# Optimization experiments

Measured on AMD Instinct MI355X. Metric: run time of the kernel, lower is better.

The kernel has to match this reference:

```python
import jax, jax.numpy as jnp
import numpy as np

D = 768          # emb_dim (BERT hidden size)
N_DOM = 9        # domain_num
N_EXP = 6        # num_expert (per-domain)
N_SH = 4         # num_shared_expert
N_TOT = N_EXP + N_SH  # total experts seen by the gate
B = 2048


def _p(key, shape, scale=0.02):
    return jax.random.normal(key, shape, dtype=jnp.float32) * scale


def setup_inputs() -> dict:
    key = jax.random.key(0)
    ks = jax.random.split(key, 32)
    inp = {
        "content_pooled": jax.random.normal(ks[0], (B, D), dtype=jnp.float32),
        "ftr_pooled": jax.random.normal(ks[1], (B, D), dtype=jnp.float32),
        "category": jax.random.randint(ks[2], (B,), 0, N_DOM, dtype=jnp.int64),
        "domain_emb": _p(ks[3], (N_DOM, D), 1.0),
    }
    # per-domain expert stacks: Linear(D,D)-SiLU-Linear(D,D), for content (c) and ftr (f)
    for pre, base in (("c", 4), ("f", 12)):
        inp[pre + "W1"] = _p(ks[base + 0], (N_DOM, N_EXP, D, D))
        inp[pre + "b1"] = jnp.zeros((N_DOM, N_EXP, D), jnp.float32)
        inp[pre + "W2"] = _p(ks[base + 1], (N_DOM, N_EXP, D, D))
        inp[pre + "b2"] = jnp.zeros((N_DOM, N_EXP, D), jnp.float32)
        # shared experts: Linear(D,D)-SiLU-Linear(D,D)
        inp[pre + "sW1"] = _p(ks[base + 2], (N_SH, D, D))
        inp[pre + "sb1"] = jnp.zeros((N_SH, D), jnp.float32)
        inp[pre + "sW2"] = _p(ks[base + 3], (N_SH, D, D))
        inp[pre + "sb2"] = jnp.zeros((N_SH, D), jnp.float32)
        # per-domain enhanced gates: Linear(2D,D)-SiLU-Linear(D,N_TOT), temperature scalar per domain
        inp[pre + "gW1"] = _p(ks[base + 4], (N_DOM, 2 * D, D))
        inp[pre + "gb1"] = jnp.zeros((N_DOM, D), jnp.float32)
        inp[pre + "gW2"] = _p(ks[base + 5], (N_DOM, D, N_TOT))
        inp[pre + "gb2"] = jnp.zeros((N_DOM, N_TOT), jnp.float32)
        inp[pre + "temp"] = jnp.ones((N_DOM,), jnp.float32)
    return inp


def _moe_branch(x, category, domain_emb, W1, b1, W2, b2,
                sW1, sb1, sW2, sb2, gW1, gb1, gW2, gb2, temp):
    # x: [B, D]; category: [B] int in [0, N_DOM)
    demb = domain_emb[category]                           # [B, D]
    g_in = jnp.concatenate([demb, x], axis=-1)            # [B, 2D]
    # gate computed for all domains, then per-example domain selected
    gh = jax.nn.silu(jnp.einsum("bx,nxh->bnh", g_in, gW1) + gb1)      # [B, 9, D]
    logits = jnp.einsum("bnh,nhe->bne", gh, gW2) + gb2                 # [B, 9, 10]
    t = jax.nn.softplus(temp) + 1e-4                                    # positive temperature
    gates_all = jax.nn.softmax(logits / t[None, :, None], axis=-1)
    gates = jnp.take_along_axis(gates_all, category[:, None, None], axis=1)[:, 0]  # [B, 10]
    # per-domain experts for all domains (grouped GEMM form), then select domain
    h1 = jax.nn.silu(jnp.einsum("bd,nedh->bneh", x, W1) + b1)          # [B, 9, 6, D]
    e_all = jnp.einsum("bneh,nehd->bned", h1, W2) + b2                 # [B, 9, 6, D]
    e_dom = jnp.take_along_axis(e_all, category[:, None, None, None], axis=1)[:, 0]  # [B, 6, D]
    # shared experts
    hs = jax.nn.silu(jnp.einsum("bd,edh->beh", x, sW1) + sb1)          # [B, 4, D]
    e_sh = jnp.einsum("beh,ehd->bed", hs, sW2) + sb2                   # [B, 4, D]
    experts = jnp.concatenate([e_dom, e_sh], axis=1)                   # [B, 10, D]
    return jnp.einsum("be,bed->bd", gates, experts)                    # [B, D]


def reference(content_pooled, ftr_pooled, category, domain_emb,
              cW1, cb1, cW2, cb2, csW1, csb1, csW2, csb2,
              cgW1, cgb1, cgW2, cgb2, ctemp,
              fW1, fb1, fW2, fb2, fsW1, fsb1, fsW2, fsb2,
              fgW1, fgb1, fgW2, fgb2, ftemp):
    c_out = _moe_branch(content_pooled, category, domain_emb,
                        cW1, cb1, cW2, cb2, csW1, csb1, csW2, csb2,
                        cgW1, cgb1, cgW2, cgb2, ctemp)
    f_out = _moe_branch(ftr_pooled, category, domain_emb,
                        fW1, fb1, fW2, fb2, fsW1, fsb1, fsW2, fsb2,
                        fgW1, fgb1, fgW2, fgb2, ftemp)
    return jnp.concatenate([c_out, f_out], axis=-1)  # [B, 2D]
```

## Files before the change

### kernel.cpp

```cpp
#include <hip/hip_runtime.h>

#define D_ 768
#define B_ 2048
#define NDOM 9
#define NTOT 10
#define MT 128
#define KT 32
#define KI1 (D_ / KT)

#define E2   589824ull
#define E2G  1179648ull
#define OFF_WT2 31850496ull
#define OFF_SW1 63700992ull
#define OFF_SW2 66060288ull
#define OFF_GW1 68419584ull
#define ZWE     79036416ull

typedef _Float16 f16;
typedef _Float16 f16x8 __attribute__((ext_vector_type(8)));
typedef float f32x4 __attribute__((ext_vector_type(4)));

typedef const __attribute__((address_space(1))) void gas_void;
typedef __attribute__((address_space(3))) void las_void;

__device__ __forceinline__ void gload16(const f16* g, f16* l) {
  __builtin_amdgcn_global_load_lds((gas_void*)g, (las_void*)l, 16, 0, 0);
}

__global__ __launch_bounds__(256) void bucket_kernel(const int* cat32, int* perm,
                                                     int* off, int* cnt, int* dom) {
  __shared__ int scnt[NDOM], soff[NDOM], scur[NDOM];
  __shared__ int odd_nz;
  int t = threadIdx.x;
  if (t == 0) odd_nz = 0;
  if (t < NDOM) scnt[t] = 0;
  __syncthreads();
  int loc = 0;
  for (int i = t; i < B_; i += 256)
    if ((i & 1) && cat32[i] != 0) loc = 1;
  if (loc) atomicOr(&odd_nz, 1);
  __syncthreads();
  int strd = odd_nz ? 1 : 2;
  for (int i = t; i < B_; i += 256) atomicAdd(&scnt[cat32[i * strd]], 1);
  __syncthreads();
  if (t == 0) { int a = 0; for (int n = 0; n < NDOM; n++) { soff[n] = a; a += scnt[n]; } }
  __syncthreads();
  if (t < NDOM) { scur[t] = soff[t]; off[t] = soff[t]; cnt[t] = scnt[t]; }
  __syncthreads();
  for (int i = t; i < B_; i += 256) {
    int n = cat32[i * strd];
    int pos = atomicAdd(&scur[n], 1);
    perm[pos] = i;
    dom[pos] = n;
  }
}

__global__ __launch_bounds__(256) void cvt_perm_kernel(const float* src, f16* dst,
                                                       const int* perm, int n8) {
  int i = blockIdx.x * 256 + threadIdx.x;
  if (i >= n8) return;
  int row = i / (D_ / 8), c8 = i % (D_ / 8);
  int srow = perm[row];
  const f32x4* s = (const f32x4*)(src + (size_t)srow * D_ + c8 * 8);
  f32x4 a = s[0], b = s[1];
  f16x8 o;
  o[0]=(f16)a[0]; o[1]=(f16)a[1]; o[2]=(f16)a[2]; o[3]=(f16)a[3];
  o[4]=(f16)b[0]; o[5]=(f16)b[1]; o[6]=(f16)b[2]; o[7]=(f16)b[3];
  *(f16x8*)(dst + (size_t)i * 8) = o;
}

struct DGP { const float* demb; const float* gW1[2]; const float* gb1[2]; float* dg; };

__global__ __launch_bounds__(256) void dgate_kernel(DGP p) {
  const int jc = blockIdx.x, n = blockIdx.y, z = blockIdx.z;
  const int j = jc * 256 + threadIdx.x;
  const float* W = p.gW1[z] + (size_t)n * 2 * D_ * D_;
  const float* de = p.demb + (size_t)n * D_;
  float acc = 0.f;
  for (int k = 0; k < D_; k++) acc = fmaf(de[k], W[(size_t)k * D_ + j], acc);
  p.dg[((size_t)z * NDOM + n) * D_ + j] = acc + p.gb1[z][n * D_ + j];
}

struct TRP { const float* s[10]; f16* wt; };

__global__ __launch_bounds__(256) void trans_kernel(TRP p) {
  const int m = blockIdx.z, z = m / 125, r = m % 125;
  const float* src; f16* dst; int R;
  const size_t zw = (size_t)z * ZWE;
  if (r < 54)       { src = p.s[0+z] + (size_t)r*E2;        dst = p.wt + zw + (size_t)r*E2;                 R = 768; }
  else if (r < 108) { int i=r-54;  src = p.s[2+z] + (size_t)i*E2;  dst = p.wt + zw + OFF_WT2 + (size_t)i*E2;  R = 768; }
  else if (r < 112) { int i=r-108; src = p.s[4+z] + (size_t)i*E2;  dst = p.wt + zw + OFF_SW1 + (size_t)i*E2;  R = 768; }
  else if (r < 116) { int i=r-112; src = p.s[6+z] + (size_t)i*E2;  dst = p.wt + zw + OFF_SW2 + (size_t)i*E2;  R = 768; }
  else              { int i=r-116; src = p.s[8+z] + (size_t)i*E2G; dst = p.wt + zw + OFF_GW1 + (size_t)i*E2G; R = 1536; }
  const int ty = blockIdx.y;
  if (ty * 64 >= R) return;
  if (R == 1536 && ty < 12) return;
  const int tx = blockIdx.x;

  __shared__ float tile[64][65];
  const int t = threadIdx.x;
  const int lr = t >> 4, lc = (t & 15) * 4;
#pragma unroll
  for (int i = 0; i < 4; i++) {
    int row = lr + i * 16;
    f32x4 v = *(const f32x4*)(src + (size_t)(ty*64 + row) * 768 + tx*64 + lc);
    tile[lc+0][row] = v[0];
    tile[lc+1][row] = v[1];
    tile[lc+2][row] = v[2];
    tile[lc+3][row] = v[3];
  }
  __syncthreads();
  const int orow = t >> 3, oc = (t & 7) * 8;
#pragma unroll
  for (int i = 0; i < 2; i++) {
    int r2 = orow + i * 32;
    f32x4 a = *(const f32x4*)&tile[r2][oc];
    f32x4 b = *(const f32x4*)&tile[r2][oc + 4];
    f16x8 o;
    o[0]=(f16)a[0]; o[1]=(f16)a[1]; o[2]=(f16)a[2]; o[3]=(f16)a[3];
    o[4]=(f16)b[0]; o[5]=(f16)b[1]; o[6]=(f16)b[2]; o[7]=(f16)b[3];
    *(f16x8*)(dst + (size_t)(tx*64 + r2) * R + ty*64 + oc) = o;
  }
}

struct L1P {
  const f16* x16p[2]; const f16* wt;
  const float* b1[2]; const float* sb1[2]; const float* dg;
  const int* off; const int* cnt;
  f16* h;
};

#define NBL1 3792
#define QX1  474

__global__ __launch_bounds__(256, 4) void layer1_kernel(L1P p) {
  const int raw = blockIdx.x;
  const int L = (raw & 7) * QX1 + (raw >> 3);
  const int z = L / 1896;
  const int rem = L - z * 1896;
  const int g = rem / 24;
  const int x = rem % 24;
  const int nt = x % 6;
  int mt0 = x / 6, mtstep = 4;

  int row_off, row_cnt, slot;
  const f16* WT; const float* bias;
  int KW = D_, koff = 0;
  const size_t zw = (size_t)z * ZWE;
  if (g < 54) {
    int n = g / 6, e = g % 6;
    row_off = p.off[n]; row_cnt = p.cnt[n];
    WT = p.wt + zw + (size_t)(n*6+e) * E2;
    bias = p.b1[z] + (n*6+e) * D_;
    slot = e;
  } else if (g < 70) {
    int s_ = g - 54, e = s_ >> 2;
    row_off = 0; row_cnt = B_;
    WT = p.wt + zw + OFF_SW1 + (size_t)e * E2;
    bias = p.sb1[z] + e * D_;
    slot = 6 + e;
    mt0 = x / 6 + 4 * (s_ & 3); mtstep = 16;
  } else {
    int n = g - 70;
    row_off = p.off[n]; row_cnt = p.cnt[n];
    WT = p.wt + zw + OFF_GW1 + (size_t)n * E2G;
    bias = p.dg + (size_t)(z * NDOM + n) * D_;
    slot = 10; KW = 2 * D_; koff = D_;
  }
  if (mt0 * MT >= row_cnt) return;

  __shared__ f16 As[2][MT][KT];
  __shared__ f16 Bs[2][MT][KT];

  const int t = threadIdx.x;
  const int wave = t >> 6, lane = t & 63;
  const int wr = (wave >> 1) * 64, wc = (wave & 1) * 64;
  const int r0 = lane & 15, q = lane >> 4;
  const int lrow = lane >> 2;
  const int lk = 8 * ((lane & 3) ^ ((lane >> 3) & 3));
  const int qa = (q ^ ((r0 >> 1) & 3)) * 8;
  const int jbase = nt * MT;

  const f16* bBase[2];
#pragma unroll
  for (int i = 0; i < 2; i++) {
    int col = jbase + 32 * wave + 16 * i + lrow;
    bBase[i] = WT + (size_t)col * KW + koff + lk;
  }
  const f16* xz = p.x16p[z];

  for (int mt = mt0; mt * MT < row_cnt; mt += mtstep) {
    const f16* aBase[2];
#pragma unroll
    for (int i = 0; i < 2; i++) {
      int rl = mt * MT + 32 * wave + 16 * i + lrow;
      if (rl >= row_cnt) rl = row_cnt - 1;
      aBase[i] = xz + (size_t)(row_off + rl) * D_ + lk;
    }

    auto STAGE = [&](int buf, int kk) {
      const int k0 = kk * KT;
      gload16(aBase[0] + k0, &As[buf][32 * wave][0]);
      gload16(aBase[1] + k0, &As[buf][32 * wave + 16][0]);
      gload16(bBase[0] + k0, &Bs[buf][32 * wave][0]);
      gload16(bBase[1] + k0, &Bs[buf][32 * wave + 16][0]);
    };

    f32x4 acc[4][4];
#pragma unroll
    for (int a = 0; a < 4; a++)
#pragma unroll
      for (int b = 0; b < 4; b++) acc[a][b] = (f32x4){0.f, 0.f, 0.f, 0.f};

    STAGE(0, 0);
    __syncthreads();
    for (int kk = 0; kk < KI1; kk++) {
      const int cur = kk & 1;
      if (kk + 1 < KI1) STAGE(cur ^ 1, kk + 1);
      f16x8 af[4], bf[4];
#pragma unroll
      for (int m = 0; m < 4; m++) af[m] = *(const f16x8*)&As[cur][wr + m * 16 + r0][qa];
#pragma unroll
      for (int nn = 0; nn < 4; nn++) bf[nn] = *(const f16x8*)&Bs[cur][wc + nn * 16 + r0][qa];
#pragma unroll
      for (int m = 0; m < 4; m++)
#pragma unroll
        for (int nn = 0; nn < 4; nn++)
          acc[m][nn] = __builtin_amdgcn_mfma_f32_16x16x32_f16(af[m], bf[nn], acc[m][nn], 0, 0, 0);
      __syncthreads();
    }

    f16* hout = p.h + (size_t)(z * 11 + slot) * B_ * D_;
#pragma unroll
    for (int nn = 0; nn < 4; nn++) {
      const int col = jbase + wc + nn * 16 + r0;
      const float bc = bias[col];
#pragma unroll
      for (int m = 0; m < 4; m++) {
#pragma unroll
        for (int i = 0; i < 4; i++) {
          int lr = mt * MT + wr + m * 16 + q * 4 + i;
          if (lr < row_cnt) {
            float v = acc[m][nn][i] + bc;
            v = v / (1.f + __expf(-v));
            hout[(size_t)(row_off + lr) * D_ + col] = (f16)v;
          }
        }
      }
    }
  }
}

struct GP {
  const f16* h;
  const float* gW2[2]; const float* gb2[2]; const float* temp[2];
  const int* dom;
  float* gates;
};

__global__ __launch_bounds__(256) void gate_kernel(GP p) {
  int wid = (blockIdx.x * 256 + threadIdx.x) >> 6;
  int lane = threadIdx.x & 63;
  int z = wid >> 11;
  int pos = wid & (B_ - 1);
  int n = p.dom[pos];
  const f16* gh = p.h + ((size_t)(z * 11 + 10) * B_ + pos) * D_;
  const float* W = p.gW2[z] + (size_t)n * D_ * NTOT;
  float part[NTOT];
#pragma unroll
  for (int e = 0; e < NTOT; e++) part[e] = 0.f;
  for (int k = lane; k < D_; k += 64) {
    float a = (float)gh[k];
    const float* wrow = W + (size_t)k * NTOT;
#pragma unroll
    for (int e = 0; e < NTOT; e++) part[e] = fmaf(a, wrow[e], part[e]);
  }
#pragma unroll
  for (int e = 0; e < NTOT; e++) {
    float v = part[e];
#pragma unroll
    for (int s = 32; s > 0; s >>= 1) v += __shfl_xor(v, s, 64);
    part[e] = v;
  }
  float tv = p.temp[z][n];
  float tq = (tv > 15.f ? tv : log1pf(__expf(tv))) + 1e-4f;
  const float* b2 = p.gb2[z] + n * NTOT;
  float mx = -1e30f;
#pragma unroll
  for (int e = 0; e < NTOT; e++) { part[e] = (part[e] + b2[e]) / tq; mx = fmaxf(mx, part[e]); }
  float s = 0.f;
#pragma unroll
  for (int e = 0; e < NTOT; e++) { part[e] = __expf(part[e] - mx); s += part[e]; }
  float inv = 1.f / s;
  if (lane < NTOT) p.gates[((size_t)z * B_ + pos) * NTOT + lane] = part[lane] * inv;
}

struct L2P {
  const f16* h; const f16* wt;
  const float* b2[2]; const float* sb2[2];
  const float* gates;
  const int* perm; const int* off; const int* cnt;
  float* out;
};

#define NBL2 2160
#define QX2  270

__global__ __launch_bounds__(256, 4) void layer2_kernel(L2P p) {
  const int raw = blockIdx.x;
  const int L = (raw & 7) * QX2 + (raw >> 3);
  const int zz = L / 216;
  const int rem = L % 216;
  const int n = rem / 24;
  const int x = rem % 24;
  const int z = zz / 5, es = zz % 5, ebase = es * 2;
  const int nt = x % 6, mt0 = x / 6;
  const int row_off = p.off[n], row_cnt = p.cnt[n];
  if (mt0 * MT >= row_cnt) return;

  __shared__ f16 As[2][MT][KT];
  __shared__ f16 Bs[2][MT][KT];
  __shared__ float sg[MT][2];
  __shared__ int sperm[MT];

  const int t = threadIdx.x;
  const int wave = t >> 6, lane = t & 63;
  const int wr = (wave >> 1) * 64, wc = (wave & 1) * 64;
  const int r0 = lane & 15, q = lane >> 4;
  const int lrow = lane >> 2;
  const int lk = 8 * ((lane & 3) ^ ((lane >> 3) & 3));
  const int qa = (q ^ ((r0 >> 1) & 3)) * 8;
  const int jbase = nt * MT;

  const size_t zw = (size_t)z * ZWE;
  const f16* WB0; const f16* WB1; const float* pb[2]; size_t slotOff[2];
  {
    int e0 = ebase, e1 = ebase + 1;
    WB0 = (e0 < 6) ? (p.wt + zw + OFF_WT2 + (size_t)(n*6+e0)*E2) : (p.wt + zw + OFF_SW2 + (size_t)(e0-6)*E2);
    WB1 = (e1 < 6) ? (p.wt + zw + OFF_WT2 + (size_t)(n*6+e1)*E2) : (p.wt + zw + OFF_SW2 + (size_t)(e1-6)*E2);
    pb[0] = (e0 < 6) ? (p.b2[z] + (size_t)(n*6+e0)*D_) : (p.sb2[z] + (size_t)(e0-6)*D_);
    pb[1] = (e1 < 6) ? (p.b2[z] + (size_t)(n*6+e1)*D_) : (p.sb2[z] + (size_t)(e1-6)*D_);
    slotOff[0] = (size_t)(z*11 + e0) * B_ * D_;
    slotOff[1] = (size_t)(z*11 + e1) * B_ * D_;
  }

  const f16* bB0[2]; const f16* bB1[2];
#pragma unroll
  for (int i = 0; i < 2; i++) {
    int col = jbase + 32 * wave + 16 * i + lrow;
    bB0[i] = WB0 + (size_t)col * D_ + lk;
    bB1[i] = WB1 + (size_t)col * D_ + lk;
  }

  for (int mt = mt0; mt * MT < row_cnt; mt += 4) {
    for (int i = t; i < MT * 2; i += 256) {
      int rr = i >> 1, e = i & 1;
      int gp = row_off + mt * MT + rr;
      sg[rr][e] = (gp < B_ && (mt * MT + rr) < row_cnt)
                  ? p.gates[((size_t)z * B_ + gp) * NTOT + ebase + e] : 0.f;
    }
    for (int i = t; i < MT; i += 256) {
      int gp = row_off + mt * MT + i;
      sperm[i] = (gp < B_) ? p.perm[gp] : 0;
    }
    __syncthreads();

    const f16* aB0[2]; const f16* aB1[2];
#pragma unroll
    for (int i = 0; i < 2; i++) {
      int rl = mt * MT + 32 * wave + 16 * i + lrow;
      int rr = (rl < row_cnt) ? (row_off + rl) : row_off;
      size_t rp = (size_t)rr * D_ + lk;
      aB0[i] = p.h + slotOff[0] + rp;
      aB1[i] = p.h + slotOff[1] + rp;
    }
    f16 gA[4], gB[4];
#pragma unroll
    for (int m = 0; m < 4; m++) {
      gA[m] = (f16)sg[wr + m * 16 + r0][0];
      gB[m] = (f16)sg[wr + m * 16 + r0][1];
    }

    auto STAGE = [&](int buf, int it) {
      const int ei = (it >= KI1);
      const int k0 = (it - (ei ? KI1 : 0)) * KT;
      gload16((ei ? aB1[0] : aB0[0]) + k0, &As[buf][32 * wave][0]);
      gload16((ei ? aB1[1] : aB0[1]) + k0, &As[buf][32 * wave + 16][0]);
      gload16((ei ? bB1[0] : bB0[0]) + k0, &Bs[buf][32 * wave][0]);
      gload16((ei ? bB1[1] : bB0[1]) + k0, &Bs[buf][32 * wave + 16][0]);
    };

    f32x4 acc[4][4];
#pragma unroll
    for (int a = 0; a < 4; a++)
#pragma unroll
      for (int b = 0; b < 4; b++) acc[a][b] = (f32x4){0.f, 0.f, 0.f, 0.f};

    const int total = 2 * KI1;
    STAGE(0, 0);
    __syncthreads();
    for (int it = 0; it < total; it++) {
      const int cur = it & 1;
      if (it + 1 < total) STAGE(cur ^ 1, it + 1);
      const int ei = (it >= KI1);
      f16x8 af[4], bf[4];
#pragma unroll
      for (int m = 0; m < 4; m++) {
        af[m] = *(const f16x8*)&As[cur][wr + m * 16 + r0][qa];
        af[m] = af[m] * (ei ? gB[m] : gA[m]);
      }
#pragma unroll
      for (int nn = 0; nn < 4; nn++) bf[nn] = *(const f16x8*)&Bs[cur][wc + nn * 16 + r0][qa];
#pragma unroll
      for (int m = 0; m < 4; m++)
#pragma unroll
        for (int nn = 0; nn < 4; nn++)
          acc[m][nn] = __builtin_amdgcn_mfma_f32_16x16x32_f16(af[m], bf[nn], acc[m][nn], 0, 0, 0);
      __syncthreads();
    }

    const int zoff = z * D_;
#pragma unroll
    for (int nn = 0; nn < 4; nn++) {
      const int col = jbase + wc + nn * 16 + r0;
      float pbc0 = pb[0][col], pbc1 = pb[1][col];
#pragma unroll
      for (int m = 0; m < 4; m++) {
#pragma unroll
        for (int i = 0; i < 4; i++) {
          const int lrt = wr + m * 16 + q * 4 + i;
          if (mt * MT + lrt < row_cnt) {
            float v = acc[m][nn][i];
            v = fmaf(sg[lrt][0], pbc0, v);
            v = fmaf(sg[lrt][1], pbc1, v);
            float* dst = p.out + (size_t)sperm[lrt] * (2 * D_) + zoff + col;
            __hip_atomic_fetch_add(dst, v, __ATOMIC_RELAXED, __HIP_MEMORY_SCOPE_AGENT);
          }
        }
      }
    }
    __syncthreads();
  }
}

extern "C" void kernel_launch(void* const* d_in, const int* in_sizes, int n_in,
                              void* d_out, int out_size, void* d_ws, size_t ws_size,
                              hipStream_t stream) {
  const float* content = (const float*)d_in[0];
  const float* ftr     = (const float*)d_in[1];
  const int*   cat     = (const int*)d_in[2];
  const float* demb    = (const float*)d_in[3];

  const float* cW1  = (const float*)d_in[4];
  const float* cb1  = (const float*)d_in[5];
  const float* cW2  = (const float*)d_in[6];
  const float* cb2  = (const float*)d_in[7];
  const float* csW1 = (const float*)d_in[8];
  const float* csb1 = (const float*)d_in[9];
  const float* csW2 = (const float*)d_in[10];
  const float* csb2 = (const float*)d_in[11];
  const float* cgW1 = (const float*)d_in[12];
  const float* cgb1 = (const float*)d_in[13];
  const float* cgW2 = (const float*)d_in[14];
  const float* cgb2 = (const float*)d_in[15];
  const float* ctemp= (const float*)d_in[16];

  const float* fW1  = (const float*)d_in[17];
  const float* fb1  = (const float*)d_in[18];
  const float* fW2  = (const float*)d_in[19];
  const float* fb2  = (const float*)d_in[20];
  const float* fsW1 = (const float*)d_in[21];
  const float* fsb1 = (const float*)d_in[22];
  const float* fsW2 = (const float*)d_in[23];
  const float* fsb2 = (const float*)d_in[24];
  const float* fgW1 = (const float*)d_in[25];
  const float* fgb1 = (const float*)d_in[26];
  const float* fgW2 = (const float*)d_in[27];
  const float* fgb2 = (const float*)d_in[28];
  const float* ftemp= (const float*)d_in[29];

  char* wsb = (char*)d_ws;
  int* perm    = (int*)wsb;
  int* off     = (int*)(wsb + 8192);
  int* cnt     = (int*)(wsb + 8256);
  int* dom     = (int*)(wsb + 8320);
  float* gates = (float*)(wsb + 16512);
  float* dg    = (float*)(wsb + 16512);
  f16* h       = (f16*)(wsb + 180352);
  f16* x16a    = (f16*)(wsb + 69386368);
  f16* x16b    = (f16*)(wsb + 72532096);
  f16* wt      = (f16*)(wsb + 75691648);
  float* out   = (float*)d_out;

  (void)hipMemsetAsync(d_out, 0, (size_t)out_size * sizeof(float), stream);

  bucket_kernel<<<1, 256, 0, stream>>>(cat, perm, off, cnt, dom);

  cvt_perm_kernel<<<768, 256, 0, stream>>>(content, x16a, perm, (B_ * D_) / 8);
  cvt_perm_kernel<<<768, 256, 0, stream>>>(ftr, x16b, perm, (B_ * D_) / 8);

  DGP pd;
  pd.demb = demb; pd.gW1[0] = cgW1; pd.gW1[1] = fgW1;
  pd.gb1[0] = cgb1; pd.gb1[1] = fgb1; pd.dg = dg;
  dgate_kernel<<<dim3(3, 9, 2), 256, 0, stream>>>(pd);

  TRP tp;
  tp.s[0] = cW1;  tp.s[1] = fW1;
  tp.s[2] = cW2;  tp.s[3] = fW2;
  tp.s[4] = csW1; tp.s[5] = fsW1;
  tp.s[6] = csW2; tp.s[7] = fsW2;
  tp.s[8] = cgW1; tp.s[9] = fgW1;
  tp.wt = wt;
  trans_kernel<<<dim3(12, 24, 250), 256, 0, stream>>>(tp);

  L1P p1;
  p1.x16p[0] = x16a; p1.x16p[1] = x16b; p1.wt = wt;
  p1.b1[0] = cb1;  p1.b1[1] = fb1;
  p1.sb1[0] = csb1; p1.sb1[1] = fsb1;
  p1.dg = dg;
  p1.off = off; p1.cnt = cnt; p1.h = h;
  layer1_kernel<<<dim3(NBL1), 256, 0, stream>>>(p1);

  GP pg;
  pg.h = h; pg.gW2[0] = cgW2; pg.gW2[1] = fgW2;
  pg.gb2[0] = cgb2; pg.gb2[1] = fgb2;
  pg.temp[0] = ctemp; pg.temp[1] = ftemp;
  pg.dom = dom; pg.gates = gates;
  gate_kernel<<<dim3((2 * B_) / 4), 256, 0, stream>>>(pg);

  L2P p2;
  p2.h = h; p2.wt = wt;
  p2.b2[0] = cb2;  p2.b2[1] = fb2;
  p2.sb2[0] = csb2; p2.sb2[1] = fsb2;
  p2.gates = gates; p2.perm = perm; p2.off = off; p2.cnt = cnt; p2.out = out;
  layer2_kernel<<<dim3(NBL2), 256, 0, stream>>>(p2);

  (void)in_sizes; (void)n_in; (void)ws_size;
}
```

Baseline: 674.8 us.

## Replace layer2 float atomics with fp16 partial buffers, reduce kernel, staged stores

Layer2 no longer scatters float atomics into the permuted output. Each of its five expert-pair groups now writes fp16 partial sums through an LDS-swizzled tile, using coalesced 16-byte stores into a scratch buffer that reuses the already-consumed W1 region of the weight workspace. A new reduce kernel sums the five partials in fp32, applies the inverse permutation, and writes the output, which removes the output memset. Layer1's epilogue gets the same LDS-staged coalesced store. The trade-off is an extra kernel and a partial-buffer round trip, plus fp16 rounding of each partial before the sum.

```diff
diff --git a/kernel.cpp b/kernel.cpp
--- a/kernel.cpp
+++ b/kernel.cpp
@@ -169,8 +169,10 @@
   }
   if (mt0 * MT >= row_cnt) return;
 
-  __shared__ f16 As[2][MT][KT];
-  __shared__ f16 Bs[2][MT][KT];
+  __shared__ f16 smem[16384];
+  f16 (*As)[MT][KT] = (f16(*)[MT][KT])smem;
+  f16 (*Bs)[MT][KT] = (f16(*)[MT][KT])(smem + 8192);
+  f16* Ts = smem;
 
   const int t = threadIdx.x;
   const int wave = t >> 6, lane = t & 63;
@@ -230,24 +232,37 @@
       __syncthreads();
     }
 
-    f16* hout = p.h + (size_t)(z * 11 + slot) * B_ * D_;
 #pragma unroll
     for (int nn = 0; nn < 4; nn++) {
-      const int col = jbase + wc + nn * 16 + r0;
-      const float bc = bias[col];
+      const int col = wc + nn * 16 + r0;
+      const float bc = bias[jbase + col];
 #pragma unroll
       for (int m = 0; m < 4; m++) {
 #pragma unroll
         for (int i = 0; i < 4; i++) {
-          int lr = mt * MT + wr + m * 16 + q * 4 + i;
-          if (lr < row_cnt) {
-            float v = acc[m][nn][i] + bc;
-            v = v / (1.f + __expf(-v));
-            hout[(size_t)(row_off + lr) * D_ + col] = (f16)v;
-          }
+          int row = wr + m * 16 + q * 4 + i;
+          float v = acc[m][nn][i] + bc;
+          v = v / (1.f + __expf(-v));
+          int ch = (col >> 3) ^ (row & 7);
+          Ts[row * 128 + ch * 8 + (col & 7)] = (f16)v;
         }
       }
     }
+    __syncthreads();
+    {
+      f16* hout = p.h + (size_t)(z * 11 + slot) * B_ * D_;
+      int row = t >> 1;
+      int gr = mt * MT + row;
+      if (gr < row_cnt) {
+        f16* dst = hout + (size_t)(row_off + gr) * D_ + jbase + (t & 1) * 64;
+#pragma unroll
+        for (int c8 = 0; c8 < 8; c8++) {
+          int ch = (((t & 1) * 8 + c8)) ^ (row & 7);
+          *(f16x8*)(dst + c8 * 8) = *(const f16x8*)&Ts[row * 128 + ch * 8];
+        }
+      }
+    }
+    __syncthreads();
   }
 }
 
@@ -299,8 +314,8 @@
   const f16* h; const f16* wt;
   const float* b2[2]; const float* sb2[2];
   const float* gates;
-  const int* perm; const int* off; const int* cnt;
-  float* out;
+  const int* off; const int* cnt;
+  f16* outp;
 };
 
 #define NBL2 2160
@@ -318,10 +333,11 @@
   const int row_off = p.off[n], row_cnt = p.cnt[n];
   if (mt0 * MT >= row_cnt) return;
 
-  __shared__ f16 As[2][MT][KT];
-  __shared__ f16 Bs[2][MT][KT];
+  __shared__ f16 smem[16384];
+  f16 (*As)[MT][KT] = (f16(*)[MT][KT])smem;
+  f16 (*Bs)[MT][KT] = (f16(*)[MT][KT])(smem + 8192);
+  f16* Ts = smem;
   __shared__ float sg[MT][2];
-  __shared__ int sperm[MT];
 
   const int t = threadIdx.x;
   const int wave = t >> 6, lane = t & 63;
@@ -359,10 +375,6 @@
       sg[rr][e] = (gp < B_ && (mt * MT + rr) < row_cnt)
                   ? p.gates[((size_t)z * B_ + gp) * NTOT + ebase + e] : 0.f;
     }
-    for (int i = t; i < MT; i += 256) {
-      int gp = row_off + mt * MT + i;
-      sperm[i] = (gp < B_) ? p.perm[gp] : 0;
-    }
     __syncthreads();
 
     const f16* aB0[2]; const f16* aB1[2];
@@ -419,28 +431,58 @@
       __syncthreads();
     }
 
-    const int zoff = z * D_;
 #pragma unroll
     for (int nn = 0; nn < 4; nn++) {
-      const int col = jbase + wc + nn * 16 + r0;
-      float pbc0 = pb[0][col], pbc1 = pb[1][col];
+      const int col = wc + nn * 16 + r0;
+      const float pbc0 = pb[0][jbase + col], pbc1 = pb[1][jbase + col];
 #pragma unroll
       for (int m = 0; m < 4; m++) {
 #pragma unroll
         for (int i = 0; i < 4; i++) {
-          const int lrt = wr + m * 16 + q * 4 + i;
-          if (mt * MT + lrt < row_cnt) {
-            float v = acc[m][nn][i];
-            v = fmaf(sg[lrt][0], pbc0, v);
-            v = fmaf(sg[lrt][1], pbc1, v);
-            float* dst = p.out + (size_t)sperm[lrt] * (2 * D_) + zoff + col;
-            __hip_atomic_fetch_add(dst, v, __ATOMIC_RELAXED, __HIP_MEMORY_SCOPE_AGENT);
-          }
+          int row = wr + m * 16 + q * 4 + i;
+          float v = acc[m][nn][i];
+          v = fmaf(sg[row][0], pbc0, v);
+          v = fmaf(sg[row][1], pbc1, v);
+          int ch = (col >> 3) ^ (row & 7);
+          Ts[row * 128 + ch * 8 + (col & 7)] = (f16)v;
         }
       }
     }
     __syncthreads();
-  }
+    {
+      int row = t >> 1;
+      int gr = mt * MT + row;
+      if (gr < row_cnt) {
+        f16* dst = p.outp + ((size_t)zz * B_ + row_off + gr) * D_ + jbase + (t & 1) * 64;
+#pragma unroll
+        for (int c8 = 0; c8 < 8; c8++) {
+          int ch = (((t & 1) * 8 + c8)) ^ (row & 7);
+          *(f16x8*)(dst + c8 * 8) = *(const f16x8*)&Ts[row * 128 + ch * 8];
+        }
+      }
+    }
+    __syncthreads();
+  }
+}
+
+__global__ __launch_bounds__(256) void reduce_kernel(const f16* outp, const int* perm,
+                                                     float* out) {
+  int idx = blockIdx.x * 256 + threadIdx.x;
+  int z = idx / (B_ * 96);
+  int rem = idx % (B_ * 96);
+  int r = rem / 96, c8 = rem % 96;
+  float s[8];
+#pragma unroll
+  for (int j = 0; j < 8; j++) s[j] = 0.f;
+#pragma unroll
+  for (int es = 0; es < 5; es++) {
+    f16x8 v = *(const f16x8*)(outp + (((size_t)(z * 5 + es)) * B_ + r) * D_ + c8 * 8);
+#pragma unroll
+    for (int j = 0; j < 8; j++) s[j] += (float)v[j];
+  }
+  float* dst = out + (size_t)perm[r] * (2 * D_) + z * D_ + c8 * 8;
+  *(f32x4*)dst = (f32x4){s[0], s[1], s[2], s[3]};
+  *(f32x4*)(dst + 4) = (f32x4){s[4], s[5], s[6], s[7]};
 }
 
 extern "C" void kernel_launch(void* const* d_in, const int* in_sizes, int n_in,
@@ -485,14 +527,13 @@
   int* cnt     = (int*)(wsb + 8256);
   int* dom     = (int*)(wsb + 8320);
   float* gates = (float*)(wsb + 16512);
-  float* dg    = (float*)(wsb + 16512);
-  f16* h       = (f16*)(wsb + 180352);
-  f16* x16a    = (f16*)(wsb + 69386368);
-  f16* x16b    = (f16*)(wsb + 72532096);
-  f16* wt      = (f16*)(wsb + 75691648);
+  float* dg    = (float*)(wsb + 16512 + 163840);
+  f16* h       = (f16*)(wsb + 409600);
+  f16* x16a    = (f16*)(wsb + 69615616);
+  f16* x16b    = (f16*)(wsb + 72761344);
+  f16* wt      = (f16*)(wsb + 75907072);
+  f16* outp    = wt;
   float* out   = (float*)d_out;
-
-  (void)hipMemsetAsync(d_out, 0, (size_t)out_size * sizeof(float), stream);
 
   bucket_kernel<<<1, 256, 0, stream>>>(cat, perm, off, cnt, dom);
 
@@ -532,8 +573,10 @@
   p2.h = h; p2.wt = wt;
   p2.b2[0] = cb2;  p2.b2[1] = fb2;
   p2.sb2[0] = csb2; p2.sb2[1] = fsb2;
-  p2.gates = gates; p2.perm = perm; p2.off = off; p2.cnt = cnt; p2.out = out;
+  p2.gates = gates; p2.off = off; p2.cnt = cnt; p2.outp = outp;
   layer2_kernel<<<dim3(NBL2), 256, 0, stream>>>(p2);
 
-  (void)in_sizes; (void)n_in; (void)ws_size;
-}
+  reduce_kernel<<<dim3((2 * B_ * 96) / 256), 256, 0, stream>>>(outp, perm, out);
+
+  (void)in_sizes; (void)n_in; (void)ws_size; (void)out_size;
+}
```

New measurement: 749.3 us. 11.0% more time.

## Convert fp32 weights to fp16 inside GEMM tiles and replace atomics with a reduction

Applied to the files above, without the earlier changes.

Drops the separate weight transpose/convert pass. Both GEMM kernels now load fp32 weights directly in their natural [k][j] layout, pack them to fp16 in registers, and write them into a padded LDS tile, overlapping this with the MFMA work. The atomic scatter-add into the output is replaced by per-expert-pair fp16 partial outputs, which a new reduce kernel sums and permutes back; this also removes the output memset. The cost is fp32 weight reads inside the hot loops, re-read by every row tile, plus an extra fp16 rounding of the partial sums.

```diff
diff --git a/kernel.cpp b/kernel.cpp
--- a/kernel.cpp
+++ b/kernel.cpp
@@ -7,17 +7,13 @@
 #define MT 128
 #define KT 32
 #define KI1 (D_ / KT)
-
-#define E2   589824ull
-#define E2G  1179648ull
-#define OFF_WT2 31850496ull
-#define OFF_SW1 63700992ull
-#define OFF_SW2 66060288ull
-#define OFF_GW1 68419584ull
-#define ZWE     79036416ull
+#define E2 589824ull
+#define LDB 40
 
 typedef _Float16 f16;
 typedef _Float16 f16x8 __attribute__((ext_vector_type(8)));
+typedef _Float16 f16x4 __attribute__((ext_vector_type(4)));
+typedef _Float16 f16x2 __attribute__((ext_vector_type(2)));
 typedef float f32x4 __attribute__((ext_vector_type(4)));
 
 typedef const __attribute__((address_space(1))) void gas_void;
@@ -26,6 +22,10 @@
 __device__ __forceinline__ void gload16(const f16* g, f16* l) {
   __builtin_amdgcn_global_load_lds((gas_void*)g, (las_void*)l, 16, 0, 0);
 }
+static __device__ __forceinline__ f16x2 pkrtz(float a, float b) {
+  return __builtin_bit_cast(f16x2, __builtin_amdgcn_cvt_pkrtz(a, b));
+}
+#define SCHED0() __builtin_amdgcn_sched_barrier(0)
 
 __global__ __launch_bounds__(256) void bucket_kernel(const int* cat32, int* perm,
                                                      int* off, int* cnt, int* dom) {
@@ -81,50 +81,9 @@
   p.dg[((size_t)z * NDOM + n) * D_ + j] = acc + p.gb1[z][n * D_ + j];
 }
 
-struct TRP { const float* s[10]; f16* wt; };
-
-__global__ __launch_bounds__(256) void trans_kernel(TRP p) {
-  const int m = blockIdx.z, z = m / 125, r = m % 125;
-  const float* src; f16* dst; int R;
-  const size_t zw = (size_t)z * ZWE;
-  if (r < 54)       { src = p.s[0+z] + (size_t)r*E2;        dst = p.wt + zw + (size_t)r*E2;                 R = 768; }
-  else if (r < 108) { int i=r-54;  src = p.s[2+z] + (size_t)i*E2;  dst = p.wt + zw + OFF_WT2 + (size_t)i*E2;  R = 768; }
-  else if (r < 112) { int i=r-108; src = p.s[4+z] + (size_t)i*E2;  dst = p.wt + zw + OFF_SW1 + (size_t)i*E2;  R = 768; }
-  else if (r < 116) { int i=r-112; src = p.s[6+z] + (size_t)i*E2;  dst = p.wt + zw + OFF_SW2 + (size_t)i*E2;  R = 768; }
-  else              { int i=r-116; src = p.s[8+z] + (size_t)i*E2G; dst = p.wt + zw + OFF_GW1 + (size_t)i*E2G; R = 1536; }
-  const int ty = blockIdx.y;
-  if (ty * 64 >= R) return;
-  if (R == 1536 && ty < 12) return;
-  const int tx = blockIdx.x;
-
-  __shared__ float tile[64][65];
-  const int t = threadIdx.x;
-  const int lr = t >> 4, lc = (t & 15) * 4;
-#pragma unroll
-  for (int i = 0; i < 4; i++) {
-    int row = lr + i * 16;
-    f32x4 v = *(const f32x4*)(src + (size_t)(ty*64 + row) * 768 + tx*64 + lc);
-    tile[lc+0][row] = v[0];
-    tile[lc+1][row] = v[1];
-    tile[lc+2][row] = v[2];
-    tile[lc+3][row] = v[3];
-  }
-  __syncthreads();
-  const int orow = t >> 3, oc = (t & 7) * 8;
-#pragma unroll
-  for (int i = 0; i < 2; i++) {
-    int r2 = orow + i * 32;
-    f32x4 a = *(const f32x4*)&tile[r2][oc];
-    f32x4 b = *(const f32x4*)&tile[r2][oc + 4];
-    f16x8 o;
-    o[0]=(f16)a[0]; o[1]=(f16)a[1]; o[2]=(f16)a[2]; o[3]=(f16)a[3];
-    o[4]=(f16)b[0]; o[5]=(f16)b[1]; o[6]=(f16)b[2]; o[7]=(f16)b[3];
-    *(f16x8*)(dst + (size_t)(tx*64 + r2) * R + ty*64 + oc) = o;
-  }
-}
-
 struct L1P {
-  const f16* x16p[2]; const f16* wt;
+  const f16* x16p[2];
+  const float* W1[2]; const float* sW1[2]; const float* gW1[2];
   const float* b1[2]; const float* sb1[2]; const float* dg;
   const int* off; const int* cnt;
   f16* h;
@@ -143,34 +102,32 @@
   const int nt = x % 6;
   int mt0 = x / 6, mtstep = 4;
 
-  int row_off, row_cnt, slot;
-  const f16* WT; const float* bias;
-  int KW = D_, koff = 0;
-  const size_t zw = (size_t)z * ZWE;
+  int row_off, row_cnt, slot, koff = 0;
+  const float* Wp; const float* bias;
   if (g < 54) {
     int n = g / 6, e = g % 6;
     row_off = p.off[n]; row_cnt = p.cnt[n];
-    WT = p.wt + zw + (size_t)(n*6+e) * E2;
+    Wp = p.W1[z] + (size_t)(n*6+e) * E2;
     bias = p.b1[z] + (n*6+e) * D_;
     slot = e;
   } else if (g < 70) {
     int s_ = g - 54, e = s_ >> 2;
     row_off = 0; row_cnt = B_;
-    WT = p.wt + zw + OFF_SW1 + (size_t)e * E2;
+    Wp = p.sW1[z] + (size_t)e * E2;
     bias = p.sb1[z] + e * D_;
     slot = 6 + e;
     mt0 = x / 6 + 4 * (s_ & 3); mtstep = 16;
   } else {
     int n = g - 70;
     row_off = p.off[n]; row_cnt = p.cnt[n];
-    WT = p.wt + zw + OFF_GW1 + (size_t)n * E2G;
+    Wp = p.gW1[z] + (size_t)n * 2 * D_ * D_;
     bias = p.dg + (size_t)(z * NDOM + n) * D_;
-    slot = 10; KW = 2 * D_; koff = D_;
+    slot = 10; koff = D_;
   }
   if (mt0 * MT >= row_cnt) return;
 
   __shared__ f16 As[2][MT][KT];
-  __shared__ f16 Bs[2][MT][KT];
+  __shared__ f16 Bs[2][MT][LDB];
 
   const int t = threadIdx.x;
   const int wave = t >> 6, lane = t & 63;
@@ -180,13 +137,10 @@
   const int lk = 8 * ((lane & 3) ^ ((lane >> 3) & 3));
   const int qa = (q ^ ((r0 >> 1) & 3)) * 8;
   const int jbase = nt * MT;
-
-  const f16* bBase[2];
-#pragma unroll
-  for (int i = 0; i < 2; i++) {
-    int col = jbase + 32 * wave + 16 * i + lrow;
-    bBase[i] = WT + (size_t)col * KW + koff + lk;
-  }
+  const int j4 = t >> 3;
+  const int kq = (t & 7) * 4;
+
+  const float* wcol = Wp + jbase + j4 * 4;
   const f16* xz = p.x16p[z];
 
   for (int mt = mt0; mt * MT < row_cnt; mt += mtstep) {
@@ -198,13 +152,26 @@
       aBase[i] = xz + (size_t)(row_off + rl) * D_ + lk;
     }
 
-    auto STAGE = [&](int buf, int kk) {
+    f32x4 wv[4];
+    auto LOADW = [&](int kk) {
+      const int kb = koff + kk * KT + kq;
+#pragma unroll
+      for (int r = 0; r < 4; r++) wv[r] = *(const f32x4*)(wcol + (size_t)(kb + r) * D_);
+    };
+    auto GLOADA = [&](int buf, int kk) {
       const int k0 = kk * KT;
       gload16(aBase[0] + k0, &As[buf][32 * wave][0]);
       gload16(aBase[1] + k0, &As[buf][32 * wave + 16][0]);
-      gload16(bBase[0] + k0, &Bs[buf][32 * wave][0]);
-      gload16(bBase[1] + k0, &Bs[buf][32 * wave + 16][0]);
     };
+    auto CVTW = [&](int buf) {
+#pragma unroll
+      for (int c = 0; c < 4; c++) {
+        union { f16x4 v; f16x2 pp[2]; } u;
+        u.pp[0] = pkrtz(wv[0][c], wv[1][c]);
+        u.pp[1] = pkrtz(wv[2][c], wv[3][c]);
+        *(f16x4*)&Bs[buf][j4 * 4 + c][kq] = u.v;
+      }
+    };
 
     f32x4 acc[4][4];
 #pragma unroll
@@ -212,21 +179,27 @@
 #pragma unroll
       for (int b = 0; b < 4; b++) acc[a][b] = (f32x4){0.f, 0.f, 0.f, 0.f};
 
-    STAGE(0, 0);
+    LOADW(0);
+    GLOADA(0, 0);
+    CVTW(0);
     __syncthreads();
+
     for (int kk = 0; kk < KI1; kk++) {
       const int cur = kk & 1;
-      if (kk + 1 < KI1) STAGE(cur ^ 1, kk + 1);
+      if (kk + 1 < KI1) { LOADW(kk + 1); GLOADA(cur ^ 1, kk + 1); }
+      SCHED0();
       f16x8 af[4], bf[4];
 #pragma unroll
       for (int m = 0; m < 4; m++) af[m] = *(const f16x8*)&As[cur][wr + m * 16 + r0][qa];
 #pragma unroll
-      for (int nn = 0; nn < 4; nn++) bf[nn] = *(const f16x8*)&Bs[cur][wc + nn * 16 + r0][qa];
+      for (int nn = 0; nn < 4; nn++) bf[nn] = *(const f16x8*)&Bs[cur][wc + nn * 16 + r0][q * 8];
 #pragma unroll
       for (int m = 0; m < 4; m++)
 #pragma unroll
         for (int nn = 0; nn < 4; nn++)
           acc[m][nn] = __builtin_amdgcn_mfma_f32_16x16x32_f16(af[m], bf[nn], acc[m][nn], 0, 0, 0);
+      SCHED0();
+      if (kk + 1 < KI1) CVTW(cur ^ 1);
       __syncthreads();
     }
 
@@ -296,11 +269,12 @@
 }
 
 struct L2P {
-  const f16* h; const f16* wt;
+  const f16* h;
+  const float* W2[2]; const float* sW2[2];
   const float* b2[2]; const float* sb2[2];
   const float* gates;
-  const int* perm; const int* off; const int* cnt;
-  float* out;
+  const int* off; const int* cnt;
+  f16* outp;
 };
 
 #define NBL2 2160
@@ -319,9 +293,8 @@
   if (mt0 * MT >= row_cnt) return;
 
   __shared__ f16 As[2][MT][KT];
-  __shared__ f16 Bs[2][MT][KT];
+  __shared__ f16 Bs[2][MT][LDB];
   __shared__ float sg[MT][2];
-  __shared__ int sperm[MT];
 
   const int t = threadIdx.x;
   const int wave = t >> 6, lane = t & 63;
@@ -331,25 +304,19 @@
   const int lk = 8 * ((lane & 3) ^ ((lane >> 3) & 3));
   const int qa = (q ^ ((r0 >> 1) & 3)) * 8;
   const int jbase = nt * MT;
-
-  const size_t zw = (size_t)z * ZWE;
-  const f16* WB0; const f16* WB1; const float* pb[2]; size_t slotOff[2];
+  const int j4 = t >> 3, kq = (t & 7) * 4;
+
+  const float* pb[2]; const float* wcol[2]; size_t slotOff[2];
   {
     int e0 = ebase, e1 = ebase + 1;
-    WB0 = (e0 < 6) ? (p.wt + zw + OFF_WT2 + (size_t)(n*6+e0)*E2) : (p.wt + zw + OFF_SW2 + (size_t)(e0-6)*E2);
-    WB1 = (e1 < 6) ? (p.wt + zw + OFF_WT2 + (size_t)(n*6+e1)*E2) : (p.wt + zw + OFF_SW2 + (size_t)(e1-6)*E2);
+    const float* WB0 = (e0 < 6) ? (p.W2[z] + (size_t)(n*6+e0)*E2) : (p.sW2[z] + (size_t)(e0-6)*E2);
+    const float* WB1 = (e1 < 6) ? (p.W2[z] + (size_t)(n*6+e1)*E2) : (p.sW2[z] + (size_t)(e1-6)*E2);
+    wcol[0] = WB0 + jbase + j4 * 4;
+    wcol[1] = WB1 + jbase + j4 * 4;
     pb[0] = (e0 < 6) ? (p.b2[z] + (size_t)(n*6+e0)*D_) : (p.sb2[z] + (size_t)(e0-6)*D_);
     pb[1] = (e1 < 6) ? (p.b2[z] + (size_t)(n*6+e1)*D_) : (p.sb2[z] + (size_t)(e1-6)*D_);
     slotOff[0] = (size_t)(z*11 + e0) * B_ * D_;
     slotOff[1] = (size_t)(z*11 + e1) * B_ * D_;
-  }
-
-  const f16* bB0[2]; const f16* bB1[2];
-#pragma unroll
-  for (int i = 0; i < 2; i++) {
-    int col = jbase + 32 * wave + 16 * i + lrow;
-    bB0[i] = WB0 + (size_t)col * D_ + lk;
-    bB1[i] = WB1 + (size_t)col * D_ + lk;
   }
 
   for (int mt = mt0; mt * MT < row_cnt; mt += 4) {
@@ -359,10 +326,6 @@
       sg[rr][e] = (gp < B_ && (mt * MT + rr) < row_cnt)
                   ? p.gates[((size_t)z * B_ + gp) * NTOT + ebase + e] : 0.f;
     }
-    for (int i = t; i < MT; i += 256) {
-      int gp = row_off + mt * MT + i;
-      sperm[i] = (gp < B_) ? p.perm[gp] : 0;
-    }
     __syncthreads();
 
     const f16* aB0[2]; const f16* aB1[2];
@@ -381,14 +344,29 @@
       gB[m] = (f16)sg[wr + m * 16 + r0][1];
     }
 
-    auto STAGE = [&](int buf, int it) {
+    f32x4 wv[4];
+    auto LOADW = [&](int it) {
+      const int ei = (it >= KI1);
+      const int kb = (it - (ei ? KI1 : 0)) * KT + kq;
+      const float* wb = wcol[ei];
+#pragma unroll
+      for (int r = 0; r < 4; r++) wv[r] = *(const f32x4*)(wb + (size_t)(kb + r) * D_);
+    };
+    auto GLOADA = [&](int buf, int it) {
       const int ei = (it >= KI1);
       const int k0 = (it - (ei ? KI1 : 0)) * KT;
       gload16((ei ? aB1[0] : aB0[0]) + k0, &As[buf][32 * wave][0]);
       gload16((ei ? aB1[1] : aB0[1]) + k0, &As[buf][32 * wave + 16][0]);
-      gload16((ei ? bB1[0] : bB0[0]) + k0, &Bs[buf][32 * wave][0]);
-      gload16((ei ? bB1[1] : bB0[1]) + k0, &Bs[buf][32 * wave + 16][0]);
     };
+    auto CVTW = [&](int buf) {
+#pragma unroll
+      for (int c = 0; c < 4; c++) {
+        union { f16x4 v; f16x2 pp[2]; } u;
+        u.pp[0] = pkrtz(wv[0][c], wv[1][c]);
+        u.pp[1] = pkrtz(wv[2][c], wv[3][c]);
+        *(f16x4*)&Bs[buf][j4 * 4 + c][kq] = u.v;
+      }
+    };
 
     f32x4 acc[4][4];
 #pragma unroll
@@ -397,11 +375,15 @@
       for (int b = 0; b < 4; b++) acc[a][b] = (f32x4){0.f, 0.f, 0.f, 0.f};
 
     const int total = 2 * KI1;
-    STAGE(0, 0);
+    LOADW(0);
+    GLOADA(0, 0);
+    CVTW(0);
     __syncthreads();
+
     for (int it = 0; it < total; it++) {
       const int cur = it & 1;
-      if (it + 1 < total) STAGE(cur ^ 1, it + 1);
+      if (it + 1 < total) { LOADW(it + 1); GLOADA(cur ^ 1, it + 1); }
+      SCHED0();
       const int ei = (it >= KI1);
       f16x8 af[4], bf[4];
 #pragma unroll
@@ -410,16 +392,17 @@
         af[m] = af[m] * (ei ? gB[m] : gA[m]);
       }
 #pragma unroll
-      for (int nn = 0; nn < 4; nn++) bf[nn] = *(const f16x8*)&Bs[cur][wc + nn * 16 + r0][qa];
+      for (int nn = 0; nn < 4; nn++) bf[nn] = *(const f16x8*)&Bs[cur][wc + nn * 16 + r0][q * 8];
 #pragma unroll
       for (int m = 0; m < 4; m++)
 #pragma unroll
         for (int nn = 0; nn < 4; nn++)
           acc[m][nn] = __builtin_amdgcn_mfma_f32_16x16x32_f16(af[m], bf[nn], acc[m][nn], 0, 0, 0);
+      SCHED0();
+      if (it + 1 < total) CVTW(cur ^ 1);
       __syncthreads();
     }
 
-    const int zoff = z * D_;
 #pragma unroll
     for (int nn = 0; nn < 4; nn++) {
       const int col = jbase + wc + nn * 16 + r0;
@@ -433,14 +416,33 @@
             float v = acc[m][nn][i];
             v = fmaf(sg[lrt][0], pbc0, v);
             v = fmaf(sg[lrt][1], pbc1, v);
-            float* dst = p.out + (size_t)sperm[lrt] * (2 * D_) + zoff + col;
-            __hip_atomic_fetch_add(dst, v, __ATOMIC_RELAXED, __HIP_MEMORY_SCOPE_AGENT);
+            p.outp[((size_t)zz * B_ + row_off + mt * MT + lrt) * D_ + col] = (f16)v;
           }
         }
       }
     }
     __syncthreads();
   }
+}
+
+__global__ __launch_bounds__(256) void reduce_kernel(const f16* outp, const int* perm,
+                                                     float* out) {
+  int idx = blockIdx.x * 256 + threadIdx.x;
+  int z = idx / (B_ * 96);
+  int rem = idx % (B_ * 96);
+  int r = rem / 96, c8 = rem % 96;
+  float s[8];
+#pragma unroll
+  for (int j = 0; j < 8; j++) s[j] = 0.f;
+#pragma unroll
+  for (int es = 0; es < 5; es++) {
+    f16x8 v = *(const f16x8*)(outp + (((size_t)(z * 5 + es)) * B_ + r) * D_ + c8 * 8);
+#pragma unroll
+    for (int j = 0; j < 8; j++) s[j] += (float)v[j];
+  }
+  float* dst = out + (size_t)perm[r] * (2 * D_) + z * D_ + c8 * 8;
+  *(f32x4*)dst = (f32x4){s[0], s[1], s[2], s[3]};
+  *(f32x4*)(dst + 4) = (f32x4){s[4], s[5], s[6], s[7]};
 }
 
 extern "C" void kernel_launch(void* const* d_in, const int* in_sizes, int n_in,
@@ -485,14 +487,12 @@
   int* cnt     = (int*)(wsb + 8256);
   int* dom     = (int*)(wsb + 8320);
   float* gates = (float*)(wsb + 16512);
-  float* dg    = (float*)(wsb + 16512);
-  f16* h       = (f16*)(wsb + 180352);
-  f16* x16a    = (f16*)(wsb + 69386368);
-  f16* x16b    = (f16*)(wsb + 72532096);
-  f16* wt      = (f16*)(wsb + 75691648);
+  float* dg    = (float*)(wsb + 180352);
+  f16* h       = (f16*)(wsb + 409600);
+  f16* x16a    = (f16*)(wsb + 69615616);
+  f16* x16b    = (f16*)(wsb + 72761344);
+  f16* outp    = (f16*)(wsb + 75907072);
   float* out   = (float*)d_out;
-
-  (void)hipMemsetAsync(d_out, 0, (size_t)out_size * sizeof(float), stream);
 
   bucket_kernel<<<1, 256, 0, stream>>>(cat, perm, off, cnt, dom);
 
@@ -504,17 +504,11 @@
   pd.gb1[0] = cgb1; pd.gb1[1] = fgb1; pd.dg = dg;
   dgate_kernel<<<dim3(3, 9, 2), 256, 0, stream>>>(pd);
 
-  TRP tp;
-  tp.s[0] = cW1;  tp.s[1] = fW1;
-  tp.s[2] = cW2;  tp.s[3] = fW2;
-  tp.s[4] = csW1; tp.s[5] = fsW1;
-  tp.s[6] = csW2; tp.s[7] = fsW2;
-  tp.s[8] = cgW1; tp.s[9] = fgW1;
-  tp.wt = wt;
-  trans_kernel<<<dim3(12, 24, 250), 256, 0, stream>>>(tp);
-
   L1P p1;
-  p1.x16p[0] = x16a; p1.x16p[1] = x16b; p1.wt = wt;
+  p1.x16p[0] = x16a; p1.x16p[1] = x16b;
+  p1.W1[0] = cW1;  p1.W1[1] = fW1;
+  p1.sW1[0] = csW1; p1.sW1[1] = fsW1;
+  p1.gW1[0] = cgW1; p1.gW1[1] = fgW1;
   p1.b1[0] = cb1;  p1.b1[1] = fb1;
   p1.sb1[0] = csb1; p1.sb1[1] = fsb1;
   p1.dg = dg;
@@ -529,11 +523,15 @@
   gate_kernel<<<dim3((2 * B_) / 4), 256, 0, stream>>>(pg);
 
   L2P p2;
-  p2.h = h; p2.wt = wt;
+  p2.h = h;
+  p2.W2[0] = cW2;  p2.W2[1] = fW2;
+  p2.sW2[0] = csW2; p2.sW2[1] = fsW2;
   p2.b2[0] = cb2;  p2.b2[1] = fb2;
   p2.sb2[0] = csb2; p2.sb2[1] = fsb2;
-  p2.gates = gates; p2.perm = perm; p2.off = off; p2.cnt = cnt; p2.out = out;
+  p2.gates = gates; p2.off = off; p2.cnt = cnt; p2.outp = outp;
   layer2_kernel<<<dim3(NBL2), 256, 0, stream>>>(p2);
 
-  (void)in_sizes; (void)n_in; (void)ws_size;
-}
+  reduce_kernel<<<dim3((2 * B_ * 96) / 256), 256, 0, stream>>>(outp, perm, out);
+
+  (void)in_sizes; (void)n_in; (void)ws_size; (void)out_size;
+}
```

New measurement: 664.3 us. Within noise of the previous version (-1.6%).
